# Performance work log

Measured on AMD Instinct MI355X. Metric: run time of the kernel, lower is better.

## Reference

```python
import jax, jax.numpy as jnp
import numpy as np

B, L, D_MODEL, N_HEAD, D_K, D_V, VOCAB = 2, 1024, 512, 8, 64, 64, 64
TEMP = float(np.sqrt(D_K))
LN_EPS = 1e-5


def setup_inputs() -> dict:
    key = jax.random.key(0)
    ks = jax.random.split(key, 24)
    inp = {}
    inp['q'] = jax.random.normal(ks[0], (B, L, D_MODEL), jnp.float32)
    inp['k'] = jax.random.normal(ks[1], (B, L, D_MODEL), jnp.float32)
    inp['v'] = jax.random.normal(ks[2], (B, L, D_MODEL), jnp.float32)
    inp['mask'] = jax.random.uniform(ks[3], (B, L, L)) < 0.1
    # tf_f1 carries -1 (padding) positions; its sign defines tf_mask for ALL five features
    inp['tf_f1'] = jax.random.randint(ks[4], (B, L, L), -1, VOCAB, jnp.int32)
    inp['tf_f2'] = jax.random.randint(ks[5], (B, L, L), 0, VOCAB, jnp.int32)
    inp['tf_f3'] = jax.random.randint(ks[6], (B, L, L), 0, VOCAB, jnp.int32)
    inp['tf_f4'] = jax.random.randint(ks[7], (B, L, L), 0, VOCAB, jnp.int32)
    inp['tf_f5'] = jax.random.randint(ks[8], (B, L, L), 0, VOCAB, jnp.int32)
    s_qk = np.sqrt(2.0 / (D_MODEL + D_K))
    s_v = np.sqrt(2.0 / (D_MODEL + D_V))
    inp['w_q'] = jax.random.normal(ks[9], (D_MODEL, N_HEAD * D_K), jnp.float32) * s_qk
    inp['b_q'] = jnp.zeros((N_HEAD * D_K,), jnp.float32)
    inp['w_k'] = jax.random.normal(ks[10], (D_MODEL, N_HEAD * D_K), jnp.float32) * s_qk
    inp['b_k'] = jnp.zeros((N_HEAD * D_K,), jnp.float32)
    inp['w_v'] = jax.random.normal(ks[11], (D_MODEL, N_HEAD * D_V), jnp.float32) * s_v
    inp['b_v'] = jnp.zeros((N_HEAD * D_V,), jnp.float32)
    for i in range(5):
        inp[f'emb{i+1}'] = jax.random.normal(ks[12 + i], (VOCAB, N_HEAD), jnp.float32)
    fc_std = np.sqrt(2.0 / (N_HEAD * D_V + D_MODEL))
    inp['fc_w'] = jax.random.normal(ks[17], (N_HEAD * D_V, D_MODEL), jnp.float32) * fc_std
    inp['fc_b'] = jnp.zeros((D_MODEL,), jnp.float32)
    inp['ln_g'] = jnp.ones((D_MODEL,), jnp.float32)
    inp['ln_b'] = jnp.zeros((D_MODEL,), jnp.float32)
    return inp


def _bias(emb, tf, tf_mask):
    # (tf * mask).long() embedding lookup, zeroed where mask==0 -> [H, B, L, L]
    idx = (tf.astype(jnp.float32) * tf_mask).astype(jnp.int32)
    feat = emb[idx] * tf_mask[..., None]          # [B, L, L, H]
    return jnp.transpose(feat, (3, 0, 1, 2))      # [H, B, L, L]


def reference(q, k, v, mask, tf_f1, tf_f2, tf_f3, tf_f4, tf_f5,
              w_q, b_q, w_k, b_k, w_v, b_v,
              emb1, emb2, emb3, emb4, emb5,
              fc_w, fc_b, ln_g, ln_b):
    residual = q
    qh = (q @ w_q + b_q).reshape(B, L, N_HEAD, D_K)
    kh = (k @ w_k + b_k).reshape(B, L, N_HEAD, D_K)
    vh = (v @ w_v + b_v).reshape(B, L, N_HEAD, D_V)

    scores = jnp.einsum('blhd,bmhd->hblm', qh, kh)  # [H, B, Lq, Lk]
    tf_mask = (tf_f1 >= 0).astype(jnp.float32)      # [B, L, L] (from tf_f1 only, as in torch)
    scores = (scores
              + _bias(emb1, tf_f1, tf_mask)
              + _bias(emb2, tf_f2, tf_mask)
              + _bias(emb3, tf_f3, tf_mask)
              + _bias(emb4, tf_f4, tf_mask)
              + _bias(emb5, tf_f5, tf_mask)) / TEMP
    scores = jnp.where(mask[None], -jnp.inf, scores)
    attn = jax.nn.softmax(scores, axis=-1)          # [H, B, L, L]; dropout = identity (eval)

    out = jnp.einsum('hblm,bmhd->blhd', attn, vh).reshape(B, L, N_HEAD * D_V)
    out = out @ fc_w + fc_b                          # dropout = identity (eval)
    out = out + residual
    mu = jnp.mean(out, axis=-1, keepdims=True)
    var = jnp.mean((out - mu) ** 2, axis=-1, keepdims=True)
    out = (out - mu) * jax.lax.rsqrt(var + LN_EPS) * ln_g + ln_b
    return out, attn.reshape(N_HEAD * B, L, L)
```

## Files before the change

kernel.cpp:

```cpp
#include <hip/hip_runtime.h>
#include <math.h>

#define L_SEQ 1024
#define DMODEL 512
#define NHEAD 8
#define NB 2

typedef __attribute__((ext_vector_type(8))) short bf8;
typedef __attribute__((ext_vector_type(4))) float f4;

__device__ __forceinline__ short f2bf(float f) {
    unsigned u = __float_as_uint(f);
    unsigned r = u + 0x7FFF + ((u >> 16) & 1);
    return (short)(r >> 16);
}

__global__ __launch_bounds__(256) void cast3_bf16_kernel(
    const float* __restrict__ s0, const float* __restrict__ s1,
    const float* __restrict__ s2,
    short* __restrict__ d0, short* __restrict__ d1, short* __restrict__ d2,
    int n4)
{
    const float* src; short* dst;
    switch (blockIdx.y) {
        case 0: src = s0; dst = d0; break;
        case 1: src = s1; dst = d1; break;
        default: src = s2; dst = d2; break;
    }
    int i = blockIdx.x * 256 + threadIdx.x;
    if (i < n4) {
        float4 f = ((const float4*)src)[i];
        short4 o;
        o.x = f2bf(f.x); o.y = f2bf(f.y); o.z = f2bf(f.z); o.w = f2bf(f.w);
        ((short4*)dst)[i] = o;
    }
}

__global__ __launch_bounds__(256) void transpose_cast_kernel(
    const float* __restrict__ s0, const float* __restrict__ s1,
    const float* __restrict__ s2, const float* __restrict__ s3,
    short* __restrict__ d0, short* __restrict__ d1,
    short* __restrict__ d2, short* __restrict__ d3)
{
    const float* src; short* dst;
    switch (blockIdx.z) {
        case 0: src = s0; dst = d0; break;
        case 1: src = s1; dst = d1; break;
        case 2: src = s2; dst = d2; break;
        default: src = s3; dst = d3; break;
    }
    __shared__ float tile[32][33];
    const int tx = threadIdx.x, ty = threadIdx.y;
    const int x0 = blockIdx.x * 32, y0 = blockIdx.y * 32;
#pragma unroll
    for (int j = 0; j < 32; j += 8)
        tile[ty + j][tx] = src[(size_t)(y0 + ty + j) * 512 + x0 + tx];
    __syncthreads();
#pragma unroll
    for (int j = 0; j < 32; j += 8)
        dst[(size_t)(x0 + ty + j) * 512 + y0 + tx] = f2bf(tile[tx][ty + j]);
}

__global__ __launch_bounds__(128) void proj_gemm_kernel(
    const short* __restrict__ qb, const short* __restrict__ kb,
    const short* __restrict__ vb,
    const short* __restrict__ Wtq, const short* __restrict__ Wtk,
    const short* __restrict__ Wtv,
    const float* __restrict__ b_q, const float* __restrict__ b_k,
    const float* __restrict__ b_v,
    short* __restrict__ qh, short* __restrict__ kh, short* __restrict__ vht)
{
    const int z = blockIdx.z;
    const short* A    = (z == 0) ? qb  : (z == 1) ? kb  : vb;
    const short* Bt   = (z == 0) ? Wtq : (z == 1) ? Wtk : Wtv;
    const float* bias = (z == 0) ? b_q : (z == 1) ? b_k : b_v;

    const int w = threadIdx.x >> 6, lane = threadIdx.x & 63;
    const int lr = lane & 15, lq = lane >> 4;
    const int m_base = blockIdx.y * 32 + w * 16;
    const int n_base = blockIdx.x * 32;

    f4 acc[2];
    const f4 zero = {0.f, 0.f, 0.f, 0.f};
    acc[0] = zero; acc[1] = zero;

    for (int k0 = 0; k0 < 512; k0 += 32) {
        bf8 a = *(const bf8*)(A + (size_t)(m_base + lr) * 512 + k0 + lq * 8);
#pragma unroll
        for (int nf = 0; nf < 2; ++nf) {
            bf8 b = *(const bf8*)(Bt + (size_t)(n_base + nf * 16 + lr) * 512 + k0 + lq * 8);
            acc[nf] = __builtin_amdgcn_mfma_f32_16x16x32_bf16(a, b, acc[nf], 0, 0, 0);
        }
    }

    short* Cnat = (z == 0) ? qh : kh;
#pragma unroll
    for (int nf = 0; nf < 2; ++nf) {
        const int n = n_base + nf * 16 + lr;
        const float bv = bias[n];
        const int mrow = m_base + lq * 4;
#pragma unroll
        for (int r = 0; r < 4; ++r) {
            const float val = acc[nf][r] + bv;
            const int m = mrow + r;
            if (z < 2) {
                Cnat[(size_t)m * 512 + n] = f2bf(val);
            } else {
                const int bb = m >> 10, l = m & 1023;
                vht[((size_t)bb * 512 + n) * 1024 + l] = f2bf(val);
            }
        }
    }
}

__global__ __launch_bounds__(128) void fc_gemm_kernel(
    const short* __restrict__ A, const short* __restrict__ Bt,
    const float* __restrict__ bias, float* __restrict__ Cout)
{
    const int w = threadIdx.x >> 6, lane = threadIdx.x & 63;
    const int lr = lane & 15, lq = lane >> 4;
    const int m_base = blockIdx.y * 32 + w * 16;
    const int n_base = blockIdx.x * 32;

    f4 acc[2];
    const f4 zero = {0.f, 0.f, 0.f, 0.f};
    acc[0] = zero; acc[1] = zero;

    for (int k0 = 0; k0 < 512; k0 += 32) {
        bf8 a = *(const bf8*)(A + (size_t)(m_base + lr) * 512 + k0 + lq * 8);
#pragma unroll
        for (int nf = 0; nf < 2; ++nf) {
            bf8 b = *(const bf8*)(Bt + (size_t)(n_base + nf * 16 + lr) * 512 + k0 + lq * 8);
            acc[nf] = __builtin_amdgcn_mfma_f32_16x16x32_bf16(a, b, acc[nf], 0, 0, 0);
        }
    }

#pragma unroll
    for (int nf = 0; nf < 2; ++nf) {
        const int n = n_base + nf * 16 + lr;
        const float bv = bias[n];
        const int mrow = m_base + lq * 4;
#pragma unroll
        for (int r = 0; r < 4; ++r)
            Cout[(size_t)(mrow + r) * 512 + n] = acc[nf][r] + bv;
    }
}

__global__ __launch_bounds__(256) void scores_mfma_kernel(
    const short* __restrict__ qh, const short* __restrict__ kh,
    float* __restrict__ sc)
{
    const int z = blockIdx.z, h = z >> 1, b = z & 1;
    const int w = threadIdx.x >> 6, lane = threadIdx.x & 63;
    const int wr = w >> 1, wc = w & 1;
    const int lr = lane & 15, lq = lane >> 4;
    const int l0 = blockIdx.y * 128 + wr * 64;
    const int m0 = blockIdx.x * 128 + wc * 64;
    const int colb = h * 64 + lq * 8;
    const size_t base = (size_t)b * L_SEQ * DMODEL;

    bf8 afr[4][2], bfr[4][2];
#pragma unroll
    for (int i = 0; i < 4; ++i)
#pragma unroll
        for (int kk = 0; kk < 2; ++kk) {
            afr[i][kk] = *(const bf8*)(qh + base + (size_t)(l0 + i * 16 + lr) * 512 + colb + kk * 32);
            bfr[i][kk] = *(const bf8*)(kh + base + (size_t)(m0 + i * 16 + lr) * 512 + colb + kk * 32);
        }

    f4 acc[4][4];
    const f4 zero = {0.f, 0.f, 0.f, 0.f};
#pragma unroll
    for (int mt = 0; mt < 4; ++mt)
#pragma unroll
        for (int nt = 0; nt < 4; ++nt) acc[mt][nt] = zero;

#pragma unroll
    for (int kk = 0; kk < 2; ++kk)
#pragma unroll
        for (int mt = 0; mt < 4; ++mt)
#pragma unroll
            for (int nt = 0; nt < 4; ++nt)
                acc[mt][nt] = __builtin_amdgcn_mfma_f32_16x16x32_bf16(
                    afr[mt][kk], bfr[nt][kk], acc[mt][nt], 0, 0, 0);

    float* out = sc + (size_t)z * L_SEQ * L_SEQ;
#pragma unroll
    for (int mt = 0; mt < 4; ++mt)
#pragma unroll
        for (int nt = 0; nt < 4; ++nt)
#pragma unroll
            for (int r = 0; r < 4; ++r)
                out[(size_t)(l0 + mt * 16 + lq * 4 + r) * 1024 + m0 + nt * 16 + lr] = acc[mt][nt][r];
}

__global__ __launch_bounds__(256) void bias_softmax_kernel(
    float* __restrict__ attn,
    const int* __restrict__ mask,
    const int* __restrict__ tf1, const int* __restrict__ tf2,
    const int* __restrict__ tf3, const int* __restrict__ tf4,
    const int* __restrict__ tf5,
    const float* __restrict__ emb1, const float* __restrict__ emb2,
    const float* __restrict__ emb3, const float* __restrict__ emb4,
    const float* __restrict__ emb5)
{
    const int l = blockIdx.x, b = blockIdx.y, t = threadIdx.x;
    __shared__ float embs[5][NHEAD][64];
    __shared__ float redmx[4][NHEAD];
    __shared__ float redsm[4][NHEAD];

    const size_t rowbase = ((size_t)(b * L_SEQ + l)) * L_SEQ + (size_t)(t * 4);
    const int4 mk  = *(const int4*)(mask + rowbase);
    const int4 i1v = *(const int4*)(tf1 + rowbase);
    const int4 i2v = *(const int4*)(tf2 + rowbase);
    const int4 i3v = *(const int4*)(tf3 + rowbase);
    const int4 i4v = *(const int4*)(tf4 + rowbase);
    const int4 i5v = *(const int4*)(tf5 + rowbase);

    f4 av[NHEAD];
#pragma unroll
    for (int h = 0; h < NHEAD; ++h)
        av[h] = *(const f4*)(attn + ((size_t)(h * NB + b) * L_SEQ + l) * L_SEQ + t * 4);

    {
        const float* es[5] = {emb1, emb2, emb3, emb4, emb5};
#pragma unroll
        for (int it = 0; it < 10; ++it) {
            const int i = it * 256 + t;
            const int j = it >> 1;
            const int rem = i & 511;
            const int h = rem >> 6, idx = rem & 63;
            embs[j][h][idx] = es[j][idx * NHEAD + h];
        }
    }
    __syncthreads();

#define BIAS_FOLD(MI, I1, I2, I3, I4, I5, MK)                                   \
    {                                                                           \
        const float tfm = ((I1) >= 0) ? 1.0f : 0.0f;                            \
        const int c1 = ((I1) >= 0) ? (I1) : 0;                                  \
        _Pragma("unroll")                                                       \
        for (int h = 0; h < NHEAD; ++h) {                                       \
            const float bsum = embs[0][h][c1] + embs[1][h][I2]                  \
                             + embs[2][h][I3] + embs[3][h][I4]                  \
                             + embs[4][h][I5];                                  \
            av[h][MI] = (MK) ? -INFINITY                                        \
                             : (av[h][MI] + bsum * tfm) * 0.125f;               \
        }                                                                       \
    }

    BIAS_FOLD(0, i1v.x, i2v.x, i3v.x, i4v.x, i5v.x, mk.x)
    BIAS_FOLD(1, i1v.y, i2v.y, i3v.y, i4v.y, i5v.y, mk.y)
    BIAS_FOLD(2, i1v.z, i2v.z, i3v.z, i4v.z, i5v.z, mk.z)
    BIAS_FOLD(3, i1v.w, i2v.w, i3v.w, i4v.w, i5v.w, mk.w)
#undef BIAS_FOLD

    const int wid = t >> 6, lane = t & 63;

    float mx[NHEAD];
#pragma unroll
    for (int h = 0; h < NHEAD; ++h)
        mx[h] = fmaxf(fmaxf(av[h][0], av[h][1]), fmaxf(av[h][2], av[h][3]));
#pragma unroll
    for (int h = 0; h < NHEAD; ++h) {
#pragma unroll
        for (int off = 1; off < 64; off <<= 1)
            mx[h] = fmaxf(mx[h], __shfl_xor(mx[h], off));
    }
    if (lane == 0) {
#pragma unroll
        for (int h = 0; h < NHEAD; ++h) redmx[wid][h] = mx[h];
    }
    __syncthreads();
#pragma unroll
    for (int h = 0; h < NHEAD; ++h)
        mx[h] = fmaxf(fmaxf(redmx[0][h], redmx[1][h]),
                      fmaxf(redmx[2][h], redmx[3][h]));

    float sm[NHEAD];
#pragma unroll
    for (int h = 0; h < NHEAD; ++h) {
        f4 e;
        e[0] = __expf(av[h][0] - mx[h]);
        e[1] = __expf(av[h][1] - mx[h]);
        e[2] = __expf(av[h][2] - mx[h]);
        e[3] = __expf(av[h][3] - mx[h]);
        av[h] = e;
        sm[h] = (e[0] + e[1]) + (e[2] + e[3]);
    }
#pragma unroll
    for (int h = 0; h < NHEAD; ++h) {
#pragma unroll
        for (int off = 1; off < 64; off <<= 1)
            sm[h] += __shfl_xor(sm[h], off);
    }
    if (lane == 0) {
#pragma unroll
        for (int h = 0; h < NHEAD; ++h) redsm[wid][h] = sm[h];
    }
    __syncthreads();

#pragma unroll
    for (int h = 0; h < NHEAD; ++h) {
        const float tot = (redsm[0][h] + redsm[1][h]) + (redsm[2][h] + redsm[3][h]);
        const float inv = 1.0f / tot;
        f4 o = av[h] * inv;
        *(f4*)(attn + ((size_t)(h * NB + b) * L_SEQ + l) * L_SEQ + t * 4) = o;
    }
}

__global__ __launch_bounds__(256) void av_mfma_kernel(
    const float* __restrict__ attn, const short* __restrict__ vht,
    short* __restrict__ pv)
{
    const int z = blockIdx.y, h = z >> 1, b = z & 1;
    const int w = threadIdx.x >> 6, lane = threadIdx.x & 63;
    const int lr = lane & 15, lq = lane >> 4;
    const int l0 = blockIdx.x * 16;
    const float* Ab = attn + (size_t)z * L_SEQ * L_SEQ;
    const short* Bb = vht + ((size_t)b * 512 + h * 64) * 1024;

    f4 acc[4];
    const f4 zero = {0.f, 0.f, 0.f, 0.f};
#pragma unroll
    for (int nt = 0; nt < 4; ++nt) acc[nt] = zero;

    const int kbeg = w * 256;
    for (int k0 = kbeg; k0 < kbeg + 256; k0 += 32) {
        const float* p = Ab + (size_t)(l0 + lr) * 1024 + k0 + lq * 8;
        float4 f0 = *(const float4*)p;
        float4 f1 = *(const float4*)(p + 4);
        bf8 a;
        a[0] = f2bf(f0.x); a[1] = f2bf(f0.y); a[2] = f2bf(f0.z); a[3] = f2bf(f0.w);
        a[4] = f2bf(f1.x); a[5] = f2bf(f1.y); a[6] = f2bf(f1.z); a[7] = f2bf(f1.w);
#pragma unroll
        for (int nt = 0; nt < 4; ++nt) {
            bf8 bv = *(const bf8*)(Bb + (size_t)(nt * 16 + lr) * 1024 + k0 + lq * 8);
            acc[nt] = __builtin_amdgcn_mfma_f32_16x16x32_bf16(a, bv, acc[nt], 0, 0, 0);
        }
    }

    __shared__ float red[4][4][16][17];
#pragma unroll
    for (int nt = 0; nt < 4; ++nt)
#pragma unroll
        for (int r = 0; r < 4; ++r)
            red[w][nt][lq * 4 + r][lr] = acc[nt][r];
    __syncthreads();

    f4 sum = zero;
#pragma unroll
    for (int j = 0; j < 4; ++j)
#pragma unroll
        for (int r = 0; r < 4; ++r)
            sum[r] += red[j][w][lq * 4 + r][lr];

#pragma unroll
    for (int r = 0; r < 4; ++r)
        pv[(size_t)(b * L_SEQ + l0 + lq * 4 + r) * 512 + h * 64 + w * 16 + lr] = f2bf(sum[r]);
}

__global__ __launch_bounds__(256) void ln_kernel(
    const float* __restrict__ x, const float* __restrict__ res,
    const float* __restrict__ g, const float* __restrict__ bvec,
    float* __restrict__ out)
{
    const int row = blockIdx.x;
    const int t = threadIdx.x;
    float2 xv = ((const float2*)(x + (size_t)row * DMODEL))[t];
    float2 rv = ((const float2*)(res + (size_t)row * DMODEL))[t];
    const float a = xv.x + rv.x;
    const float c = xv.y + rv.y;
    float s = a + c, sq = a * a + c * c;
#pragma unroll
    for (int off = 32; off; off >>= 1) {
        s  += __shfl_down(s, off);
        sq += __shfl_down(sq, off);
    }
    __shared__ float ssum[4], ssq[4];
    __shared__ float smu, srs;
    const int wid = t >> 6, lane = t & 63;
    if (lane == 0) { ssum[wid] = s; ssq[wid] = sq; }
    __syncthreads();
    if (t == 0) {
        float ts = ssum[0] + ssum[1] + ssum[2] + ssum[3];
        float tq = ssq[0] + ssq[1] + ssq[2] + ssq[3];
        float mu = ts * (1.0f / DMODEL);
        float var = tq * (1.0f / DMODEL) - mu * mu;
        smu = mu;
        srs = rsqrtf(var + 1e-5f);
    }
    __syncthreads();
    const float mu = smu, rs = srs;
    float2 gv = ((const float2*)g)[t];
    float2 bv = ((const float2*)bvec)[t];
    float2 o;
    o.x = (a - mu) * rs * gv.x + bv.x;
    o.y = (c - mu) * rs * gv.y + bv.y;
    ((float2*)(out + (size_t)row * DMODEL))[t] = o;
}

extern "C" void kernel_launch(void* const* d_in, const int* in_sizes, int n_in,
                              void* d_out, int out_size, void* d_ws, size_t ws_size,
                              hipStream_t stream)
{
    const float* q    = (const float*)d_in[0];
    const float* k    = (const float*)d_in[1];
    const float* v    = (const float*)d_in[2];
    const int*   mask = (const int*)d_in[3];
    const int*   tf1  = (const int*)d_in[4];
    const int*   tf2  = (const int*)d_in[5];
    const int*   tf3  = (const int*)d_in[6];
    const int*   tf4  = (const int*)d_in[7];
    const int*   tf5  = (const int*)d_in[8];
    const float* w_q  = (const float*)d_in[9];
    const float* b_q  = (const float*)d_in[10];
    const float* w_k  = (const float*)d_in[11];
    const float* b_k  = (const float*)d_in[12];
    const float* w_v  = (const float*)d_in[13];
    const float* b_v  = (const float*)d_in[14];
    const float* emb1 = (const float*)d_in[15];
    const float* emb2 = (const float*)d_in[16];
    const float* emb3 = (const float*)d_in[17];
    const float* emb4 = (const float*)d_in[18];
    const float* emb5 = (const float*)d_in[19];
    const float* fc_w = (const float*)d_in[20];
    const float* fc_b = (const float*)d_in[21];
    const float* ln_g = (const float*)d_in[22];
    const float* ln_b = (const float*)d_in[23];

    float* out  = (float*)d_out;
    float* attn = out + (size_t)NB * L_SEQ * DMODEL;

    char* wsb = (char*)d_ws;
    short* qb   = (short*)(wsb + 0);
    short* kb   = (short*)(wsb + (2u << 20));
    short* vb   = (short*)(wsb + (4u << 20));
    short* Wtq  = (short*)(wsb + (6u << 20));
    short* Wtk  = (short*)(wsb + (6u << 20) + (512u << 10));
    short* Wtv  = (short*)(wsb + (7u << 20));
    short* Wtfc = (short*)(wsb + (7u << 20) + (512u << 10));
    short* qh   = (short*)(wsb + (8u << 20));
    short* kh   = (short*)(wsb + (10u << 20));
    short* vht  = (short*)(wsb + (12u << 20));
    short* pv   = (short*)(wsb + (14u << 20));
    float* fco  = (float*)(wsb + (16u << 20));

    const int n4 = NB * L_SEQ * DMODEL / 4;

    cast3_bf16_kernel<<<dim3(n4 / 256, 3), 256, 0, stream>>>(
        q, k, v, qb, kb, vb, n4);

    transpose_cast_kernel<<<dim3(16, 16, 4), dim3(32, 8), 0, stream>>>(
        w_q, w_k, w_v, fc_w, Wtq, Wtk, Wtv, Wtfc);

    proj_gemm_kernel<<<dim3(16, 64, 3), 128, 0, stream>>>(
        qb, kb, vb, Wtq, Wtk, Wtv, b_q, b_k, b_v, qh, kh, vht);

    scores_mfma_kernel<<<dim3(8, 8, 16), 256, 0, stream>>>(qh, kh, attn);

    bias_softmax_kernel<<<dim3(L_SEQ, NB), 256, 0, stream>>>(
        attn, mask, tf1, tf2, tf3, tf4, tf5, emb1, emb2, emb3, emb4, emb5);

    av_mfma_kernel<<<dim3(64, 16), 256, 0, stream>>>(attn, vht, pv);

    fc_gemm_kernel<<<dim3(16, 64), 128, 0, stream>>>(pv, Wtfc, fc_b, fco);

    ln_kernel<<<NB * L_SEQ, 256, 0, stream>>>(fco, q, ln_g, ln_b, out);
}
```

Baseline: 274.8 us.

## Fuse scores, bias, softmax and AV into one flash-style attention kernel

Replaces the separate scores GEMM, bias+softmax pass and AV GEMM with a single kernel. It computes QK^T twice (once for online max/sum, once to emit probabilities), adds the embedding bias from a packed per-position word, writes attn once, and feeds bf16 probabilities through LDS into the AV MFMA. A new pre-pass packs the mask and five tf indices into one 32-bit word per position. The input cast kernel is dropped by converting fp32 inputs inside the projection GEMM, and the fc output goes straight into the output buffer before in-place layer norm. This removes the fp32 score round trips through HBM at the cost of recomputing QK^T and adding an extra packing pass over the tf arrays.

```diff
diff --git a/kernel.cpp b/kernel.cpp
--- a/kernel.cpp
+++ b/kernel.cpp
@@ -15,25 +15,27 @@
     return (short)(r >> 16);
 }
 
-__global__ __launch_bounds__(256) void cast3_bf16_kernel(
-    const float* __restrict__ s0, const float* __restrict__ s1,
-    const float* __restrict__ s2,
-    short* __restrict__ d0, short* __restrict__ d1, short* __restrict__ d2,
-    int n4)
-{
-    const float* src; short* dst;
-    switch (blockIdx.y) {
-        case 0: src = s0; dst = d0; break;
-        case 1: src = s1; dst = d1; break;
-        default: src = s2; dst = d2; break;
-    }
+__global__ __launch_bounds__(256) void pack_tf_kernel(
+    const int* __restrict__ mask,
+    const int* __restrict__ tf1, const int* __restrict__ tf2,
+    const int* __restrict__ tf3, const int* __restrict__ tf4,
+    const int* __restrict__ tf5, unsigned* __restrict__ pk, int n4)
+{
     int i = blockIdx.x * 256 + threadIdx.x;
-    if (i < n4) {
-        float4 f = ((const float4*)src)[i];
-        short4 o;
-        o.x = f2bf(f.x); o.y = f2bf(f.y); o.z = f2bf(f.z); o.w = f2bf(f.w);
-        ((short4*)dst)[i] = o;
-    }
+    if (i >= n4) return;
+    const int4 mk = ((const int4*)mask)[i];
+    const int4 a1 = ((const int4*)tf1)[i];
+    const int4 a2 = ((const int4*)tf2)[i];
+    const int4 a3 = ((const int4*)tf3)[i];
+    const int4 a4 = ((const int4*)tf4)[i];
+    const int4 a5 = ((const int4*)tf5)[i];
+    uint4 o;
+#define PK(F) ((mk.F ? 0x80000000u : 0u) | ((unsigned)(a1.F + 1) << 24) \
+               | ((unsigned)a2.F << 18) | ((unsigned)a3.F << 12)        \
+               | ((unsigned)a4.F << 6) | (unsigned)a5.F)
+    o.x = PK(x); o.y = PK(y); o.z = PK(z); o.w = PK(w);
+#undef PK
+    ((uint4*)pk)[i] = o;
 }
 
 __global__ __launch_bounds__(256) void transpose_cast_kernel(
@@ -62,8 +64,8 @@
 }
 
 __global__ __launch_bounds__(128) void proj_gemm_kernel(
-    const short* __restrict__ qb, const short* __restrict__ kb,
-    const short* __restrict__ vb,
+    const float* __restrict__ q, const float* __restrict__ k,
+    const float* __restrict__ v,
     const short* __restrict__ Wtq, const short* __restrict__ Wtk,
     const short* __restrict__ Wtv,
     const float* __restrict__ b_q, const float* __restrict__ b_k,
@@ -71,7 +73,7 @@
     short* __restrict__ qh, short* __restrict__ kh, short* __restrict__ vht)
 {
     const int z = blockIdx.z;
-    const short* A    = (z == 0) ? qb  : (z == 1) ? kb  : vb;
+    const float* A    = (z == 0) ? q   : (z == 1) ? k   : v;
     const short* Bt   = (z == 0) ? Wtq : (z == 1) ? Wtk : Wtv;
     const float* bias = (z == 0) ? b_q : (z == 1) ? b_k : b_v;
 
@@ -85,7 +87,12 @@
     acc[0] = zero; acc[1] = zero;
 
     for (int k0 = 0; k0 < 512; k0 += 32) {
-        bf8 a = *(const bf8*)(A + (size_t)(m_base + lr) * 512 + k0 + lq * 8);
+        const float* p = A + (size_t)(m_base + lr) * 512 + k0 + lq * 8;
+        float4 f0 = *(const float4*)p;
+        float4 f1 = *(const float4*)(p + 4);
+        bf8 a;
+        a[0] = f2bf(f0.x); a[1] = f2bf(f0.y); a[2] = f2bf(f0.z); a[3] = f2bf(f0.w);
+        a[4] = f2bf(f1.x); a[5] = f2bf(f1.y); a[6] = f2bf(f1.z); a[7] = f2bf(f1.w);
 #pragma unroll
         for (int nf = 0; nf < 2; ++nf) {
             bf8 b = *(const bf8*)(Bt + (size_t)(n_base + nf * 16 + lr) * 512 + k0 + lq * 8);
@@ -113,6 +120,204 @@
     }
 }
 
+__global__ __launch_bounds__(512) void flash_attn_kernel(
+    const short* __restrict__ qh, const short* __restrict__ kh,
+    const short* __restrict__ vht, const unsigned* __restrict__ pk,
+    const float* __restrict__ emb1, const float* __restrict__ emb2,
+    const float* __restrict__ emb3, const float* __restrict__ emb4,
+    const float* __restrict__ emb5,
+    float* __restrict__ attn, short* __restrict__ pv)
+{
+    const int z = blockIdx.x, h = z >> 1, b = z & 1;
+    const int t = threadIdx.x;
+    const int wave = t >> 6, lane = t & 63;
+    const int wr = wave & 1, wm = wave >> 1;
+    const int lr = lane & 15, lq = lane >> 4;
+    const int l0 = blockIdx.y * 32 + wr * 16;
+    const int mbase = wm * 256;
+
+    __shared__ float embs[5][64];
+    __shared__ float red_mx[4][2][16];
+    __shared__ float red_sm[4][2][16];
+    __shared__ short plds[8][1024];
+    __shared__ float ored[4][2][16][64];
+
+    if (t < 320) {
+        const float* es[5] = {emb1, emb2, emb3, emb4, emb5};
+        embs[t >> 6][t & 63] = es[t >> 6][(t & 63) * NHEAD + h];
+    }
+
+    const short* qp = qh + ((size_t)(b * L_SEQ + l0 + lr)) * DMODEL + h * 64 + lq * 8;
+    const bf8 aq0 = *(const bf8*)qp;
+    const bf8 aq1 = *(const bf8*)(qp + 32);
+
+    const int lrow0 = l0 + lq * 4;
+    int tboff[4];
+#pragma unroll
+    for (int r = 0; r < 4; ++r)
+        tboff[r] = (b * L_SEQ + lrow0 + r) * L_SEQ + lr;
+    const short* kbp = kh + (size_t)b * L_SEQ * DMODEL + h * 64 + lq * 8;
+
+    __syncthreads();
+
+    const f4 zero = {0.f, 0.f, 0.f, 0.f};
+
+#define COMPUTE_S(m0, sv)                                                     \
+    {                                                                         \
+        f4 acc[4];                                                            \
+        acc[0] = zero; acc[1] = zero; acc[2] = zero; acc[3] = zero;           \
+        _Pragma("unroll")                                                     \
+        for (int nt = 0; nt < 4; ++nt) {                                      \
+            const short* kp = kbp + (size_t)((m0) + nt * 16 + lr) * DMODEL;   \
+            bf8 b0 = *(const bf8*)kp;                                         \
+            bf8 b1 = *(const bf8*)(kp + 32);                                  \
+            acc[nt] = __builtin_amdgcn_mfma_f32_16x16x32_bf16(aq0, b0, acc[nt], 0, 0, 0); \
+            acc[nt] = __builtin_amdgcn_mfma_f32_16x16x32_bf16(aq1, b1, acc[nt], 0, 0, 0); \
+        }                                                                     \
+        _Pragma("unroll")                                                     \
+        for (int nt = 0; nt < 4; ++nt) {                                      \
+            _Pragma("unroll")                                                 \
+            for (int r = 0; r < 4; ++r) {                                     \
+                const unsigned u = pk[tboff[r] + (m0) + nt * 16];             \
+                float sval;                                                   \
+                if (u & 0x80000000u) { sval = -INFINITY; }                    \
+                else {                                                        \
+                    const int i1m = (u >> 24) & 0x7F;                         \
+                    float bs = 0.f;                                           \
+                    if (i1m) bs = embs[0][i1m - 1] + embs[1][(u >> 18) & 63]  \
+                                + embs[2][(u >> 12) & 63]                     \
+                                + embs[3][(u >> 6) & 63] + embs[4][u & 63];   \
+                    sval = (acc[nt][r] + bs) * 0.125f;                        \
+                }                                                             \
+                sv[nt][r] = sval;                                             \
+            }                                                                 \
+        }                                                                     \
+    }
+
+    float mx[4], sm[4];
+#pragma unroll
+    for (int r = 0; r < 4; ++r) { mx[r] = -INFINITY; sm[r] = 0.f; }
+
+    for (int mt = 0; mt < 4; ++mt) {
+        const int m0 = mbase + mt * 64;
+        float sv[4][4];
+        COMPUTE_S(m0, sv);
+        float tmx[4];
+#pragma unroll
+        for (int r = 0; r < 4; ++r)
+            tmx[r] = fmaxf(fmaxf(sv[0][r], sv[1][r]), fmaxf(sv[2][r], sv[3][r]));
+#pragma unroll
+        for (int r = 0; r < 4; ++r) {
+#pragma unroll
+            for (int off = 1; off < 16; off <<= 1)
+                tmx[r] = fmaxf(tmx[r], __shfl_xor(tmx[r], off));
+        }
+        float mnew[4], tsum[4];
+#pragma unroll
+        for (int r = 0; r < 4; ++r) { mnew[r] = fmaxf(mx[r], tmx[r]); tsum[r] = 0.f; }
+#pragma unroll
+        for (int nt = 0; nt < 4; ++nt)
+#pragma unroll
+            for (int r = 0; r < 4; ++r)
+                tsum[r] += (sv[nt][r] > -INFINITY) ? __expf(sv[nt][r] - mnew[r]) : 0.f;
+#pragma unroll
+        for (int r = 0; r < 4; ++r) {
+#pragma unroll
+            for (int off = 1; off < 16; off <<= 1)
+                tsum[r] += __shfl_xor(tsum[r], off);
+        }
+#pragma unroll
+        for (int r = 0; r < 4; ++r) {
+            const float fac = (mx[r] == -INFINITY) ? 0.f : __expf(mx[r] - mnew[r]);
+            sm[r] = sm[r] * fac + tsum[r];
+            mx[r] = mnew[r];
+        }
+    }
+
+    if (lr == 0) {
+#pragma unroll
+        for (int r = 0; r < 4; ++r) {
+            red_mx[wm][wr][lq * 4 + r] = mx[r];
+            red_sm[wm][wr][lq * 4 + r] = sm[r];
+        }
+    }
+    __syncthreads();
+
+    float mfin[4], inv[4];
+#pragma unroll
+    for (int r = 0; r < 4; ++r) {
+        const int row = lq * 4 + r;
+        const float m0_ = red_mx[0][wr][row], m1_ = red_mx[1][wr][row];
+        const float m2_ = red_mx[2][wr][row], m3_ = red_mx[3][wr][row];
+        const float mf = fmaxf(fmaxf(m0_, m1_), fmaxf(m2_, m3_));
+        float s = 0.f;
+        if (m0_ > -INFINITY) s += red_sm[0][wr][row] * __expf(m0_ - mf);
+        if (m1_ > -INFINITY) s += red_sm[1][wr][row] * __expf(m1_ - mf);
+        if (m2_ > -INFINITY) s += red_sm[2][wr][row] * __expf(m2_ - mf);
+        if (m3_ > -INFINITY) s += red_sm[3][wr][row] * __expf(m3_ - mf);
+        mfin[r] = mf;
+        inv[r] = 1.0f / s;
+    }
+
+    f4 oacc[4];
+    oacc[0] = zero; oacc[1] = zero; oacc[2] = zero; oacc[3] = zero;
+    float* ap = attn + (size_t)z * L_SEQ * L_SEQ;
+    short* pbase = &plds[wave][0];
+
+    for (int mt = 0; mt < 4; ++mt) {
+        const int m0 = mbase + mt * 64;
+        float sv[4][4];
+        COMPUTE_S(m0, sv);
+#pragma unroll
+        for (int nt = 0; nt < 4; ++nt) {
+#pragma unroll
+            for (int r = 0; r < 4; ++r) {
+                const float p = (sv[nt][r] > -INFINITY)
+                                    ? __expf(sv[nt][r] - mfin[r]) * inv[r] : 0.f;
+                ap[(size_t)(lrow0 + r) * L_SEQ + m0 + nt * 16 + lr] = p;
+                const int row = lq * 4 + r, col = nt * 16 + lr;
+                const int boff = (row * 128 + col * 2) ^ ((row & 7) << 4);
+                *(short*)((char*)pbase + boff) = f2bf(p);
+            }
+        }
+        asm volatile("s_waitcnt lgkmcnt(0)" ::: "memory");
+#pragma unroll
+        for (int kk = 0; kk < 2; ++kk) {
+            const int rb = (lr * 128 + (kk * 32 + lq * 8) * 2) ^ ((lr & 7) << 4);
+            const bf8 pa = *(const bf8*)((const char*)pbase + rb);
+#pragma unroll
+            for (int ntd = 0; ntd < 4; ++ntd) {
+                const bf8 bv = *(const bf8*)(vht
+                    + ((size_t)b * DMODEL + h * 64 + ntd * 16 + lr) * L_SEQ
+                    + m0 + kk * 32 + lq * 8);
+                oacc[ntd] = __builtin_amdgcn_mfma_f32_16x16x32_bf16(pa, bv, oacc[ntd], 0, 0, 0);
+            }
+        }
+    }
+#undef COMPUTE_S
+
+#pragma unroll
+    for (int ntd = 0; ntd < 4; ++ntd)
+#pragma unroll
+        for (int r = 0; r < 4; ++r)
+            ored[wm][wr][lq * 4 + r][ntd * 16 + lr] = oacc[ntd][r];
+    __syncthreads();
+    if (wm == 0) {
+#pragma unroll
+        for (int ntd = 0; ntd < 4; ++ntd) {
+#pragma unroll
+            for (int r = 0; r < 4; ++r) {
+                const int row = lq * 4 + r;
+                const float s = ored[0][wr][row][ntd * 16 + lr]
+                              + ored[1][wr][row][ntd * 16 + lr]
+                              + ored[2][wr][row][ntd * 16 + lr]
+                              + ored[3][wr][row][ntd * 16 + lr];
+                pv[((size_t)(b * L_SEQ) + l0 + row) * 512 + h * 64 + ntd * 16 + lr] = f2bf(s);
+            }
+        }
+    }
+}
+
 __global__ __launch_bounds__(128) void fc_gemm_kernel(
     const short* __restrict__ A, const short* __restrict__ Bt,
     const float* __restrict__ bias, float* __restrict__ Cout)
@@ -144,220 +349,6 @@
         for (int r = 0; r < 4; ++r)
             Cout[(size_t)(mrow + r) * 512 + n] = acc[nf][r] + bv;
     }
-}
-
-__global__ __launch_bounds__(256) void scores_mfma_kernel(
-    const short* __restrict__ qh, const short* __restrict__ kh,
-    float* __restrict__ sc)
-{
-    const int z = blockIdx.z, h = z >> 1, b = z & 1;
-    const int w = threadIdx.x >> 6, lane = threadIdx.x & 63;
-    const int wr = w >> 1, wc = w & 1;
-    const int lr = lane & 15, lq = lane >> 4;
-    const int l0 = blockIdx.y * 128 + wr * 64;
-    const int m0 = blockIdx.x * 128 + wc * 64;
-    const int colb = h * 64 + lq * 8;
-    const size_t base = (size_t)b * L_SEQ * DMODEL;
-
-    bf8 afr[4][2], bfr[4][2];
-#pragma unroll
-    for (int i = 0; i < 4; ++i)
-#pragma unroll
-        for (int kk = 0; kk < 2; ++kk) {
-            afr[i][kk] = *(const bf8*)(qh + base + (size_t)(l0 + i * 16 + lr) * 512 + colb + kk * 32);
-            bfr[i][kk] = *(const bf8*)(kh + base + (size_t)(m0 + i * 16 + lr) * 512 + colb + kk * 32);
-        }
-
-    f4 acc[4][4];
-    const f4 zero = {0.f, 0.f, 0.f, 0.f};
-#pragma unroll
-    for (int mt = 0; mt < 4; ++mt)
-#pragma unroll
-        for (int nt = 0; nt < 4; ++nt) acc[mt][nt] = zero;
-
-#pragma unroll
-    for (int kk = 0; kk < 2; ++kk)
-#pragma unroll
-        for (int mt = 0; mt < 4; ++mt)
-#pragma unroll
-            for (int nt = 0; nt < 4; ++nt)
-                acc[mt][nt] = __builtin_amdgcn_mfma_f32_16x16x32_bf16(
-                    afr[mt][kk], bfr[nt][kk], acc[mt][nt], 0, 0, 0);
-
-    float* out = sc + (size_t)z * L_SEQ * L_SEQ;
-#pragma unroll
-    for (int mt = 0; mt < 4; ++mt)
-#pragma unroll
-        for (int nt = 0; nt < 4; ++nt)
-#pragma unroll
-            for (int r = 0; r < 4; ++r)
-                out[(size_t)(l0 + mt * 16 + lq * 4 + r) * 1024 + m0 + nt * 16 + lr] = acc[mt][nt][r];
-}
-
-__global__ __launch_bounds__(256) void bias_softmax_kernel(
-    float* __restrict__ attn,
-    const int* __restrict__ mask,
-    const int* __restrict__ tf1, const int* __restrict__ tf2,
-    const int* __restrict__ tf3, const int* __restrict__ tf4,
-    const int* __restrict__ tf5,
-    const float* __restrict__ emb1, const float* __restrict__ emb2,
-    const float* __restrict__ emb3, const float* __restrict__ emb4,
-    const float* __restrict__ emb5)
-{
-    const int l = blockIdx.x, b = blockIdx.y, t = threadIdx.x;
-    __shared__ float embs[5][NHEAD][64];
-    __shared__ float redmx[4][NHEAD];
-    __shared__ float redsm[4][NHEAD];
-
-    const size_t rowbase = ((size_t)(b * L_SEQ + l)) * L_SEQ + (size_t)(t * 4);
-    const int4 mk  = *(const int4*)(mask + rowbase);
-    const int4 i1v = *(const int4*)(tf1 + rowbase);
-    const int4 i2v = *(const int4*)(tf2 + rowbase);
-    const int4 i3v = *(const int4*)(tf3 + rowbase);
-    const int4 i4v = *(const int4*)(tf4 + rowbase);
-    const int4 i5v = *(const int4*)(tf5 + rowbase);
-
-    f4 av[NHEAD];
-#pragma unroll
-    for (int h = 0; h < NHEAD; ++h)
-        av[h] = *(const f4*)(attn + ((size_t)(h * NB + b) * L_SEQ + l) * L_SEQ + t * 4);
-
-    {
-        const float* es[5] = {emb1, emb2, emb3, emb4, emb5};
-#pragma unroll
-        for (int it = 0; it < 10; ++it) {
-            const int i = it * 256 + t;
-            const int j = it >> 1;
-            const int rem = i & 511;
-            const int h = rem >> 6, idx = rem & 63;
-            embs[j][h][idx] = es[j][idx * NHEAD + h];
-        }
-    }
-    __syncthreads();
-
-#define BIAS_FOLD(MI, I1, I2, I3, I4, I5, MK)                                   \
-    {                                                                           \
-        const float tfm = ((I1) >= 0) ? 1.0f : 0.0f;                            \
-        const int c1 = ((I1) >= 0) ? (I1) : 0;                                  \
-        _Pragma("unroll")                                                       \
-        for (int h = 0; h < NHEAD; ++h) {                                       \
-            const float bsum = embs[0][h][c1] + embs[1][h][I2]                  \
-                             + embs[2][h][I3] + embs[3][h][I4]                  \
-                             + embs[4][h][I5];                                  \
-            av[h][MI] = (MK) ? -INFINITY                                        \
-                             : (av[h][MI] + bsum * tfm) * 0.125f;               \
-        }                                                                       \
-    }
-
-    BIAS_FOLD(0, i1v.x, i2v.x, i3v.x, i4v.x, i5v.x, mk.x)
-    BIAS_FOLD(1, i1v.y, i2v.y, i3v.y, i4v.y, i5v.y, mk.y)
-    BIAS_FOLD(2, i1v.z, i2v.z, i3v.z, i4v.z, i5v.z, mk.z)
-    BIAS_FOLD(3, i1v.w, i2v.w, i3v.w, i4v.w, i5v.w, mk.w)
-#undef BIAS_FOLD
-
-    const int wid = t >> 6, lane = t & 63;
-
-    float mx[NHEAD];
-#pragma unroll
-    for (int h = 0; h < NHEAD; ++h)
-        mx[h] = fmaxf(fmaxf(av[h][0], av[h][1]), fmaxf(av[h][2], av[h][3]));
-#pragma unroll
-    for (int h = 0; h < NHEAD; ++h) {
-#pragma unroll
-        for (int off = 1; off < 64; off <<= 1)
-            mx[h] = fmaxf(mx[h], __shfl_xor(mx[h], off));
-    }
-    if (lane == 0) {
-#pragma unroll
-        for (int h = 0; h < NHEAD; ++h) redmx[wid][h] = mx[h];
-    }
-    __syncthreads();
-#pragma unroll
-    for (int h = 0; h < NHEAD; ++h)
-        mx[h] = fmaxf(fmaxf(redmx[0][h], redmx[1][h]),
-                      fmaxf(redmx[2][h], redmx[3][h]));
-
-    float sm[NHEAD];
-#pragma unroll
-    for (int h = 0; h < NHEAD; ++h) {
-        f4 e;
-        e[0] = __expf(av[h][0] - mx[h]);
-        e[1] = __expf(av[h][1] - mx[h]);
-        e[2] = __expf(av[h][2] - mx[h]);
-        e[3] = __expf(av[h][3] - mx[h]);
-        av[h] = e;
-        sm[h] = (e[0] + e[1]) + (e[2] + e[3]);
-    }
-#pragma unroll
-    for (int h = 0; h < NHEAD; ++h) {
-#pragma unroll
-        for (int off = 1; off < 64; off <<= 1)
-            sm[h] += __shfl_xor(sm[h], off);
-    }
-    if (lane == 0) {
-#pragma unroll
-        for (int h = 0; h < NHEAD; ++h) redsm[wid][h] = sm[h];
-    }
-    __syncthreads();
-
-#pragma unroll
-    for (int h = 0; h < NHEAD; ++h) {
-        const float tot = (redsm[0][h] + redsm[1][h]) + (redsm[2][h] + redsm[3][h]);
-        const float inv = 1.0f / tot;
-        f4 o = av[h] * inv;
-        *(f4*)(attn + ((size_t)(h * NB + b) * L_SEQ + l) * L_SEQ + t * 4) = o;
-    }
-}
-
-__global__ __launch_bounds__(256) void av_mfma_kernel(
-    const float* __restrict__ attn, const short* __restrict__ vht,
-    short* __restrict__ pv)
-{
-    const int z = blockIdx.y, h = z >> 1, b = z & 1;
-    const int w = threadIdx.x >> 6, lane = threadIdx.x & 63;
-    const int lr = lane & 15, lq = lane >> 4;
-    const int l0 = blockIdx.x * 16;
-    const float* Ab = attn + (size_t)z * L_SEQ * L_SEQ;
-    const short* Bb = vht + ((size_t)b * 512 + h * 64) * 1024;
-
-    f4 acc[4];
-    const f4 zero = {0.f, 0.f, 0.f, 0.f};
-#pragma unroll
-    for (int nt = 0; nt < 4; ++nt) acc[nt] = zero;
-
-    const int kbeg = w * 256;
-    for (int k0 = kbeg; k0 < kbeg + 256; k0 += 32) {
-        const float* p = Ab + (size_t)(l0 + lr) * 1024 + k0 + lq * 8;
-        float4 f0 = *(const float4*)p;
-        float4 f1 = *(const float4*)(p + 4);
-        bf8 a;
-        a[0] = f2bf(f0.x); a[1] = f2bf(f0.y); a[2] = f2bf(f0.z); a[3] = f2bf(f0.w);
-        a[4] = f2bf(f1.x); a[5] = f2bf(f1.y); a[6] = f2bf(f1.z); a[7] = f2bf(f1.w);
-#pragma unroll
-        for (int nt = 0; nt < 4; ++nt) {
-            bf8 bv = *(const bf8*)(Bb + (size_t)(nt * 16 + lr) * 1024 + k0 + lq * 8);
-            acc[nt] = __builtin_amdgcn_mfma_f32_16x16x32_bf16(a, bv, acc[nt], 0, 0, 0);
-        }
-    }
-
-    __shared__ float red[4][4][16][17];
-#pragma unroll
-    for (int nt = 0; nt < 4; ++nt)
-#pragma unroll
-        for (int r = 0; r < 4; ++r)
-            red[w][nt][lq * 4 + r][lr] = acc[nt][r];
-    __syncthreads();
-
-    f4 sum = zero;
-#pragma unroll
-    for (int j = 0; j < 4; ++j)
-#pragma unroll
-        for (int r = 0; r < 4; ++r)
-            sum[r] += red[j][w][lq * 4 + r][lr];
-
-#pragma unroll
-    for (int r = 0; r < 4; ++r)
-        pv[(size_t)(b * L_SEQ + l0 + lq * 4 + r) * 512 + h * 64 + w * 16 + lr] = f2bf(sum[r]);
 }
 
 __global__ __launch_bounds__(256) void ln_kernel(
@@ -433,38 +424,31 @@
     float* attn = out + (size_t)NB * L_SEQ * DMODEL;
 
     char* wsb = (char*)d_ws;
-    short* qb   = (short*)(wsb + 0);
-    short* kb   = (short*)(wsb + (2u << 20));
-    short* vb   = (short*)(wsb + (4u << 20));
-    short* Wtq  = (short*)(wsb + (6u << 20));
-    short* Wtk  = (short*)(wsb + (6u << 20) + (512u << 10));
-    short* Wtv  = (short*)(wsb + (7u << 20));
-    short* Wtfc = (short*)(wsb + (7u << 20) + (512u << 10));
-    short* qh   = (short*)(wsb + (8u << 20));
-    short* kh   = (short*)(wsb + (10u << 20));
-    short* vht  = (short*)(wsb + (12u << 20));
-    short* pv   = (short*)(wsb + (14u << 20));
-    float* fco  = (float*)(wsb + (16u << 20));
-
-    const int n4 = NB * L_SEQ * DMODEL / 4;
-
-    cast3_bf16_kernel<<<dim3(n4 / 256, 3), 256, 0, stream>>>(
-        q, k, v, qb, kb, vb, n4);
+    unsigned* pk = (unsigned*)(wsb + 0);
+    short* Wtq  = (short*)(wsb + (8u << 20));
+    short* Wtk  = (short*)(wsb + (8u << 20) + (512u << 10));
+    short* Wtv  = (short*)(wsb + (9u << 20));
+    short* Wtfc = (short*)(wsb + (9u << 20) + (512u << 10));
+    short* qh   = (short*)(wsb + (10u << 20));
+    short* kh   = (short*)(wsb + (12u << 20));
+    short* vht  = (short*)(wsb + (14u << 20));
+    short* pv   = (short*)(wsb + (16u << 20));
+
+    const int npk4 = NB * L_SEQ * L_SEQ / 4;
+
+    pack_tf_kernel<<<npk4 / 256, 256, 0, stream>>>(
+        mask, tf1, tf2, tf3, tf4, tf5, pk, npk4);
 
     transpose_cast_kernel<<<dim3(16, 16, 4), dim3(32, 8), 0, stream>>>(
         w_q, w_k, w_v, fc_w, Wtq, Wtk, Wtv, Wtfc);
 
     proj_gemm_kernel<<<dim3(16, 64, 3), 128, 0, stream>>>(
-        qb, kb, vb, Wtq, Wtk, Wtv, b_q, b_k, b_v, qh, kh, vht);
-
-    scores_mfma_kernel<<<dim3(8, 8, 16), 256, 0, stream>>>(qh, kh, attn);
-
-    bias_softmax_kernel<<<dim3(L_SEQ, NB), 256, 0, stream>>>(
-        attn, mask, tf1, tf2, tf3, tf4, tf5, emb1, emb2, emb3, emb4, emb5);
-
-    av_mfma_kernel<<<dim3(64, 16), 256, 0, stream>>>(attn, vht, pv);
-
-    fc_gemm_kernel<<<dim3(16, 64), 128, 0, stream>>>(pv, Wtfc, fc_b, fco);
-
-    ln_kernel<<<NB * L_SEQ, 256, 0, stream>>>(fco, q, ln_g, ln_b, out);
-}
+        q, k, v, Wtq, Wtk, Wtv, b_q, b_k, b_v, qh, kh, vht);
+
+    flash_attn_kernel<<<dim3(16, 32), 512, 0, stream>>>(
+        qh, kh, vht, pk, emb1, emb2, emb3, emb4, emb5, attn, pv);
+
+    fc_gemm_kernel<<<dim3(16, 64), 128, 0, stream>>>(pv, Wtfc, fc_b, out);
+
+    ln_kernel<<<NB * L_SEQ, 256, 0, stream>>>(out, q, ln_g, ln_b, out);
+}
```

Measured after the change: 300.7 us. +9.4%, slower.
